# Performance work log

Hardware: AMD Instinct MI355X
Metric: run time of the kernel (lower is better)

The kernel has to match this reference:

```python
import jax, jax.numpy as jnp
import numpy as np

B, H, S, D = 4, 32, 2048, 128  # batch, heads, seq_len, d_head
D_MODEL = H * D


def setup_inputs() -> dict:
    key = jax.random.key(0)
    ks = jax.random.split(key, 6)
    return {
        "query_states": jax.random.normal(ks[0], (B, H, S, D), dtype=jnp.float32),
        "key_states": jax.random.normal(ks[1], (B, H, S, D), dtype=jnp.float32),
        "value_states": jax.random.normal(ks[2], (B, H, S, D), dtype=jnp.float32),
        "local_attn_outputs": jax.random.normal(ks[3], (B, H, S, D), dtype=jnp.float32),
        "balance_factors": jax.random.normal(ks[4], (H,), dtype=jnp.float32),
        "w_o": jax.random.normal(ks[5], (D_MODEL, D_MODEL), dtype=jnp.float32) / np.sqrt(D_MODEL),
    }


def reference(query_states, key_states, value_states, local_attn_outputs, balance_factors, w_o):
    # --- compressive memory from keys/values (elu+1 feature map) ---
    phi_k = jax.nn.elu(key_states) + 1.0                                  # [B,H,S,D]
    memory = jnp.einsum("bhsk,bhsv->bhkv", phi_k, value_states)           # [B,H,D,D]
    normalization = jnp.sum(phi_k, axis=2)                                # [B,H,D]

    # --- retrieval with query feature map, normalized ---
    phi_q = jax.nn.elu(query_states) + 1.0                                # [B,H,S,D]
    retrieved = jnp.einsum("bhsk,bhkv->bhsv", phi_q, memory)              # [B,H,S,D]
    denom = jnp.einsum("bhsk,bhk->bhs", phi_q, normalization)             # [B,H,S]
    retrieved = retrieved / denom[..., None]

    # --- sigmoid-gated combine of global (memory) and local attention ---
    gw = jax.nn.sigmoid(balance_factors)[None, :, None, None]             # global weights
    lw = jax.nn.sigmoid(1.0 - balance_factors)[None, :, None, None]      # local weights
    attn = gw * retrieved + lw * local_attn_outputs                       # [B,H,S,D]

    # [B,H,S,D] -> [B,S,H*D]
    attn = jnp.transpose(attn, (0, 2, 1, 3)).reshape(B, S, H * D)
    # o_proj: bias-free Linear, y = x @ W^T
    return attn @ w_o.T
```

## Files before the change

kernel.cpp:

```cpp
#include <hip/hip_runtime.h>
#include <hip/hip_bf16.h>

#define B_ 4
#define H_ 32
#define S_ 2048
#define D_ 128
#define DM_ 4096
#define BH_ (B_*H_)
#define M_ (B_*S_)

typedef short bf16x8 __attribute__((ext_vector_type(8)));
typedef short s16x4  __attribute__((ext_vector_type(4)));
typedef float f32x4  __attribute__((ext_vector_type(4)));

__device__ __forceinline__ float phi_f(float x) {
    return x > 0.f ? x + 1.f : __expf(x);
}

__device__ __forceinline__ short f2b(float x) {
    __hip_bfloat16 h = __float2bfloat16(x);
    return *(short*)&h;
}

__device__ __forceinline__ void gl_lds16(void* lds_uniform, const void* gptr) {
    __builtin_amdgcn_global_load_lds(
        (const __attribute__((address_space(1))) void*)gptr,
        (__attribute__((address_space(3))) void*)lds_uniform,
        16, 0, 0);
}

__global__ __launch_bounds__(256) void k1_memory(
    const float* __restrict__ Kin, const float* __restrict__ Vin,
    float* __restrict__ parts, float* __restrict__ nrmP)
{
    const int split = blockIdx.x;
    const int bh = blockIdx.y;
    const int t = threadIdx.x;
    const int wave = t >> 6, lane = t & 63;
    const int lm = lane & 15, quad = lane >> 4;
    const int wm = wave >> 1, wn = wave & 1;

    __shared__ __hip_bfloat16 sVt[128*72];
    __shared__ __hip_bfloat16 sKt[128*72];

    const long base = (long)bh * S_ * D_ + (long)split * (S_/8) * D_;
    const float* Kp = Kin + base;
    const float* Vp = Vin + base;

    f32x4 acc[4][4];
#pragma unroll
    for (int i = 0; i < 4; ++i)
#pragma unroll
        for (int j = 0; j < 4; ++j) { f32x4 z = {0.f,0.f,0.f,0.f}; acc[i][j] = z; }

    float na[2][4] = {{0.f,0.f,0.f,0.f},{0.f,0.f,0.f,0.f}};

    const int si  = t & 15;
    const int dj0 = t >> 4;

    for (int c = 0; c < 4; ++c) {
        const int s0 = c*64 + si*4;
        __syncthreads();
#pragma unroll
        for (int m = 0; m < 2; ++m) {
            const int dj = dj0 + 16*m;
            const float* gK = Kp + (long)s0*D_ + dj*4;
            const float* gV = Vp + (long)s0*D_ + dj*4;
            float4 krv[4], vrv[4];
#pragma unroll
            for (int r = 0; r < 4; ++r) {
                krv[r] = *(const float4*)(gK + (long)r*D_);
                vrv[r] = *(const float4*)(gV + (long)r*D_);
            }
            const float* kf = (const float*)krv;
            const float* vf = (const float*)vrv;
#pragma unroll
            for (int cc = 0; cc < 4; ++cc) {
                float p0 = phi_f(kf[0*4+cc]), p1 = phi_f(kf[1*4+cc]);
                float p2 = phi_f(kf[2*4+cc]), p3 = phi_f(kf[3*4+cc]);
                na[m][cc] += p0 + p1 + p2 + p3;
                s16x4 pw; pw[0]=f2b(p0); pw[1]=f2b(p1); pw[2]=f2b(p2); pw[3]=f2b(p3);
                s16x4 vw; vw[0]=f2b(vf[0*4+cc]); vw[1]=f2b(vf[1*4+cc]);
                          vw[2]=f2b(vf[2*4+cc]); vw[3]=f2b(vf[3*4+cc]);
                const int d = dj*4 + cc;
                *(s16x4*)(sKt + d*72 + si*4) = pw;
                *(s16x4*)(sVt + d*72 + si*4) = vw;
            }
        }
        __syncthreads();
#pragma unroll
        for (int kh = 0; kh < 2; ++kh) {
            const int scol = kh*32 + quad*8;
            bf16x8 af[4], bfr[4];
#pragma unroll
            for (int x = 0; x < 4; ++x) {
                af[x]  = *(const bf16x8*)(sVt + (wm*64 + x*16 + lm)*72 + scol);
                bfr[x] = *(const bf16x8*)(sKt + (wn*64 + x*16 + lm)*72 + scol);
            }
#pragma unroll
            for (int mt = 0; mt < 4; ++mt)
#pragma unroll
                for (int nt = 0; nt < 4; ++nt)
                    acc[mt][nt] = __builtin_amdgcn_mfma_f32_16x16x32_bf16(
                        af[mt], bfr[nt], acc[mt][nt], 0, 0, 0);
        }
    }

#pragma unroll
    for (int m = 0; m < 2; ++m)
#pragma unroll
        for (int cc = 0; cc < 4; ++cc) {
            float v = na[m][cc];
            v += __shfl_xor(v, 1); v += __shfl_xor(v, 2);
            v += __shfl_xor(v, 4); v += __shfl_xor(v, 8);
            na[m][cc] = v;
        }
    if (si == 0) {
        float* np = nrmP + ((long)split*BH_ + bh)*D_;
        *(float4*)&np[dj0*4]      = make_float4(na[0][0], na[0][1], na[0][2], na[0][3]);
        *(float4*)&np[(dj0+16)*4] = make_float4(na[1][0], na[1][1], na[1][2], na[1][3]);
    }

    float* mp = parts + ((long)split*BH_ + bh) * (D_*D_);
#pragma unroll
    for (int mt = 0; mt < 4; ++mt)
#pragma unroll
        for (int nt = 0; nt < 4; ++nt) {
            const int kcol = wn*64 + nt*16 + lm;
#pragma unroll
            for (int r = 0; r < 4; ++r) {
                const int vrow = wm*64 + mt*16 + quad*4 + r;
                mp[vrow*D_ + kcol] = acc[mt][nt][r];
            }
        }
}

__global__ __launch_bounds__(256) void k1b_finalize(
    const float* __restrict__ parts, const float* __restrict__ nrmP,
    __hip_bfloat16* __restrict__ memTb, float* __restrict__ nrm)
{
    const int bid = blockIdx.x;
    if (bid >= 1024) {
        const int idx = (bid - 1024)*256 + threadIdx.x;
        float s = 0.f;
#pragma unroll
        for (int sp = 0; sp < 8; ++sp) s += nrmP[(long)sp*BH_*D_ + idx];
        nrm[idx] = s;
        return;
    }
    const long g = (long)bid*256 + threadIdx.x;
    const int bh  = (int)(g >> 11);
    const int rem = (int)(g & 2047);
    const int row = rem >> 4, seg = rem & 15;
    const int srcSeg = seg ^ (row & 15);
    const long sbase = (long)bh*(D_*D_) + row*D_ + srcSeg*8;

    f32x4 s0 = {0.f,0.f,0.f,0.f}, s1 = {0.f,0.f,0.f,0.f};
#pragma unroll
    for (int sp = 0; sp < 8; ++sp) {
        const float* p = parts + (long)sp*BH_*(D_*D_) + sbase;
        s0 += *(const f32x4*)p;
        s1 += *(const f32x4*)(p + 4);
    }
    bf16x8 ob;
#pragma unroll
    for (int j = 0; j < 4; ++j) { ob[j] = f2b(s0[j]); ob[4+j] = f2b(s1[j]); }
    *(bf16x8*)(memTb + g*8) = ob;
}

__global__ __launch_bounds__(256) void k2_retrieve(
    const float* __restrict__ Qin, const float* __restrict__ Lin,
    const float* __restrict__ bal,
    const __hip_bfloat16* __restrict__ memTb, const float* __restrict__ nrm,
    __hip_bfloat16* __restrict__ attnB)
{
    const int sc = blockIdx.x;
    const int bh = blockIdx.y;
    const int b = bh >> 5, h = bh & 31;
    const int t = threadIdx.x;
    const int wave = t >> 6, lane = t & 63;
    const int lm = lane & 15, quad = lane >> 4;
    const int wm = wave >> 1, wn = wave & 1;

    __shared__ char smem[128*132*4];
    __hip_bfloat16* sQ = (__hip_bfloat16*)smem;
    __hip_bfloat16* sM = (__hip_bfloat16*)(smem + 32768);
    float* sOut = (float*)smem;
    __shared__ float sDenP[128][8];
    __shared__ float sDen[128];

    const float* Qp = Qin + (long)bh*S_*D_ + (long)sc*128*D_;
    const float* Lp = Lin + (long)bh*S_*D_ + (long)sc*128*D_;
    const __hip_bfloat16* mb = memTb + (long)bh*(D_*D_);

#pragma unroll
    for (int i = 0; i < 8; ++i)
        gl_lds16((void*)(sM + (i*256 + wave*64)*8),
                 (const void*)(mb + (long)(i*256 + wave*64 + lane)*8));

    const int kq = t & 31;
    const float4 nq = *(const float4*)(nrm + bh*D_ + kq*4);
#pragma unroll
    for (int i = 0; i < 16; ++i) {
        const int idx = t + i*256;
        const int row = idx >> 5;
        float4 qv = *(const float4*)(Qp + (long)idx*4);
        float p0 = phi_f(qv.x), p1 = phi_f(qv.y), p2 = phi_f(qv.z), p3 = phi_f(qv.w);
        float part = p0*nq.x + p1*nq.y + p2*nq.z + p3*nq.w;
        part += __shfl_xor(part, 1);
        part += __shfl_xor(part, 2);
        if ((kq & 3) == 0) sDenP[row][kq >> 2] = part;
        const int seg = kq >> 1, half = kq & 1;
        const int off = row*128 + ((seg ^ (row & 15)) << 3) + half*4;
        s16x4 qw; qw[0]=f2b(p0); qw[1]=f2b(p1); qw[2]=f2b(p2); qw[3]=f2b(p3);
        *(s16x4*)(sQ + off) = qw;
    }
    __syncthreads();

    if (t < 128) {
        float d = 0.f;
#pragma unroll
        for (int j = 0; j < 8; ++j) d += sDenP[t][j];
        sDen[t] = d;
    }

    f32x4 acc[4][4];
#pragma unroll
    for (int i = 0; i < 4; ++i)
#pragma unroll
        for (int j = 0; j < 4; ++j) { f32x4 z = {0.f,0.f,0.f,0.f}; acc[i][j] = z; }

#pragma unroll
    for (int kh = 0; kh < 4; ++kh) {
        const int segk = kh*4 + quad;
        bf16x8 af[4], bfr[4];
#pragma unroll
        for (int x = 0; x < 4; ++x) {
            const int srow = wm*64 + x*16 + lm;
            af[x]  = *(const bf16x8*)(sQ + srow*128 + ((segk ^ (srow & 15)) << 3));
            const int vrow = wn*64 + x*16 + lm;
            bfr[x] = *(const bf16x8*)(sM + vrow*128 + ((segk ^ (vrow & 15)) << 3));
        }
#pragma unroll
        for (int mt = 0; mt < 4; ++mt)
#pragma unroll
            for (int nt = 0; nt < 4; ++nt)
                acc[mt][nt] = __builtin_amdgcn_mfma_f32_16x16x32_bf16(
                    af[mt], bfr[nt], acc[mt][nt], 0, 0, 0);
    }

    const float bv = bal[h];
    const float gw = 1.f/(1.f+__expf(-bv));
    const float lw = 1.f/(1.f+__expf(-(1.f-bv)));

    __syncthreads();
#pragma unroll
    for (int mt = 0; mt < 4; ++mt)
#pragma unroll
        for (int r = 0; r < 4; ++r) {
            const int srow = wm*64 + mt*16 + quad*4 + r;
            const float scale = gw / sDen[srow];
#pragma unroll
            for (int nt = 0; nt < 4; ++nt)
                sOut[srow*132 + wn*64 + nt*16 + lm] = acc[mt][nt][r]*scale;
        }
    __syncthreads();

    const int seg = t & 15;
#pragma unroll
    for (int i = 0; i < 8; ++i) {
        const int row = (t >> 4) + i*16;
        const float* Lr = Lp + (long)row*D_ + seg*8;
        const float* Or = sOut + row*132 + seg*8;
        float4 l0 = *(const float4*)Lr;
        float4 l1 = *(const float4*)(Lr + 4);
        f32x4 o0 = *(const f32x4*)Or;
        f32x4 o1 = *(const f32x4*)(Or + 4);
        bf16x8 ob;
        ob[0] = f2b(o0[0] + lw*l0.x); ob[1] = f2b(o0[1] + lw*l0.y);
        ob[2] = f2b(o0[2] + lw*l0.z); ob[3] = f2b(o0[3] + lw*l0.w);
        ob[4] = f2b(o1[0] + lw*l1.x); ob[5] = f2b(o1[1] + lw*l1.y);
        ob[6] = f2b(o1[2] + lw*l1.z); ob[7] = f2b(o1[3] + lw*l1.w);
        const long oidx = ((long)b*S_ + sc*128 + row)*DM_ + h*D_ + seg*8;
        *(bf16x8*)(attnB + oidx) = ob;
    }
}

__global__ __launch_bounds__(256) void kconv(
    const float* __restrict__ w, __hip_bfloat16* __restrict__ wb)
{
    const long base = (long)blockIdx.x*256 + threadIdx.x;
#pragma unroll
    for (int it = 0; it < 8; ++it) {
        long i = (base + (long)it*524288)*4;
        float4 f = *(const float4*)(w + i);
        __hip_bfloat16 ob[4] = {__float2bfloat16(f.x), __float2bfloat16(f.y),
                                __float2bfloat16(f.z), __float2bfloat16(f.w)};
        *(uint2*)(wb + i) = *(uint2*)ob;
    }
}

#define GBM 256
#define GBN 256
#define GBK 64
#define GNT (DM_/GBK)

__device__ __forceinline__ bf16x8 ldfrag(const __hip_bfloat16* base, int row, int k) {
    const int kk = k ^ ((row & 7) << 3);
    return *(const bf16x8*)(base + row * GBK + kk);
}

__device__ __forceinline__ void stage_half(
    const __hip_bfloat16* __restrict__ G, __hip_bfloat16* sb,
    int r0g, int kb, int wave, int lane)
{
#pragma unroll
    for (int r = 0; r < 4; ++r) {
        const int c   = r * 512 + wave * 64 + lane;
        const int row = c >> 3;
        const int ko  = ((c & 7) ^ (row & 7)) * 8;
        gl_lds16((void*)(sb + (r * 512 + wave * 64) * 8),
                 (const void*)(G + (long)(r0g + row) * DM_ + kb + ko));
    }
}

__global__ __launch_bounds__(512, 2) void k3_gemm(
    const __hip_bfloat16* __restrict__ X,
    const __hip_bfloat16* __restrict__ W,
    float* __restrict__ Y)
{
    __shared__ alignas(16) __hip_bfloat16 sA[2][GBM * GBK];
    __shared__ alignas(16) __hip_bfloat16 sB[2][GBN * GBK];

    const int tid = threadIdx.x;
    const int wave = tid >> 6, lane = tid & 63;
    const int lm = lane & 15, quad = lane >> 4;
    const int wm = wave >> 2, wn = wave & 3;

    const int orig = blockIdx.x;
    const int wg = (orig & 7) * 64 + (orig >> 3);
    const int m0 = (wg >> 4) * GBM;
    const int n0 = (wg & 15) * GBN;

    f32x4 acc[8][4];
#pragma unroll
    for (int i = 0; i < 8; ++i)
#pragma unroll
        for (int j = 0; j < 4; ++j) { f32x4 z = {0.f,0.f,0.f,0.f}; acc[i][j] = z; }

    const int ar0 = wm * 128 + lm;
    const int br0 = wn * 64 + lm;
    const int kq  = quad * 8;

    stage_half(W, sB[0], n0, 0, wave, lane);
    stage_half(X, sA[0], m0, 0, wave, lane);
    stage_half(W, sB[1], n0, GBK, wave, lane);
    stage_half(X, sA[1], m0, GBK, wave, lane);
    asm volatile("s_waitcnt vmcnt(8)" ::: "memory");
    __builtin_amdgcn_s_barrier();

    bf16x8 a[4][2], b[4][2];

    for (int t = 0; t < GNT; ++t) {
        const int cur = t & 1;
        const __hip_bfloat16* As = sA[cur];
        const __hip_bfloat16* Bs = sB[cur];

#pragma unroll
        for (int mf = 0; mf < 4; ++mf)
#pragma unroll
            for (int kh = 0; kh < 2; ++kh)
                a[mf][kh] = ldfrag(As, ar0 + mf * 16, kh * 32 + kq);
#pragma unroll
        for (int nf = 0; nf < 4; ++nf)
#pragma unroll
            for (int kh = 0; kh < 2; ++kh)
                b[nf][kh] = ldfrag(Bs, br0 + nf * 16, kh * 32 + kq);

        __builtin_amdgcn_s_setprio(1);
#pragma unroll
        for (int mf = 0; mf < 4; ++mf)
#pragma unroll
            for (int nf = 0; nf < 4; ++nf)
#pragma unroll
                for (int kh = 0; kh < 2; ++kh)
                    acc[mf][nf] = __builtin_amdgcn_mfma_f32_16x16x32_bf16(
                        a[mf][kh], b[nf][kh], acc[mf][nf], 0, 0, 0);
        __builtin_amdgcn_s_setprio(0);

#pragma unroll
        for (int mf = 0; mf < 4; ++mf)
#pragma unroll
            for (int kh = 0; kh < 2; ++kh)
                a[mf][kh] = ldfrag(As, ar0 + 64 + mf * 16, kh * 32 + kq);

        asm volatile("s_waitcnt lgkmcnt(0)" ::: "memory");
        __builtin_amdgcn_sched_barrier(0);
        __builtin_amdgcn_s_barrier();

        if (t + 2 < GNT) {
            stage_half(W, sB[cur], n0, (t + 2) * GBK, wave, lane);
            stage_half(X, sA[cur], m0, (t + 2) * GBK, wave, lane);
        }

        __builtin_amdgcn_s_setprio(1);
#pragma unroll
        for (int mf = 0; mf < 4; ++mf)
#pragma unroll
            for (int nf = 0; nf < 4; ++nf)
#pragma unroll
                for (int kh = 0; kh < 2; ++kh)
                    acc[4 + mf][nf] = __builtin_amdgcn_mfma_f32_16x16x32_bf16(
                        a[mf][kh], b[nf][kh], acc[4 + mf][nf], 0, 0, 0);
        __builtin_amdgcn_s_setprio(0);

        if (t + 2 < GNT)
            asm volatile("s_waitcnt vmcnt(8)" ::: "memory");
        else
            asm volatile("s_waitcnt vmcnt(0)" ::: "memory");
        __builtin_amdgcn_s_barrier();
    }

#pragma unroll
    for (int mf = 0; mf < 8; ++mf) {
        const int row = m0 + wm * 128 + mf * 16 + quad * 4;
#pragma unroll
        for (int nf = 0; nf < 4; ++nf) {
            const int col = n0 + wn * 64 + nf * 16 + lm;
#pragma unroll
            for (int r = 0; r < 4; ++r)
                Y[(long)(row + r) * DM_ + col] = acc[mf][nf][r];
        }
    }
}

extern "C" void kernel_launch(void* const* d_in, const int* in_sizes, int n_in,
                              void* d_out, int out_size, void* d_ws, size_t ws_size,
                              hipStream_t stream) {
    const float* Q   = (const float*)d_in[0];
    const float* K   = (const float*)d_in[1];
    const float* V   = (const float*)d_in[2];
    const float* L   = (const float*)d_in[3];
    const float* bal = (const float*)d_in[4];
    const float* Wo  = (const float*)d_in[5];
    float* Y = (float*)d_out;

    char* ws = (char*)d_ws;
    float* parts = (float*)ws;
    __hip_bfloat16* attnB = (__hip_bfloat16*)ws;
    __hip_bfloat16* woB = (__hip_bfloat16*)(ws + 67108864);
    float* nrm   = (float*)(ws + 100663296);
    __hip_bfloat16* memTb = (__hip_bfloat16*)(ws + 100728832);
    float* nrmP  = (float*)(ws + 104923136);


    k1_memory<<<dim3(8, BH_), 256, 0, stream>>>(K, V, parts, nrmP);
    k1b_finalize<<<1088, 256, 0, stream>>>(parts, nrmP, memTb, nrm);
    kconv<<<2048, 256, 0, stream>>>(Wo, woB);
    k2_retrieve<<<dim3(S_/128, BH_), 256, 0, stream>>>(Q, L, bal, memTb, nrm, attnB);
    k3_gemm<<<dim3(512), 512, 0, stream>>>(attnB, woB, Y);
}
```

Baseline: 829.6 us.

## Load W fragments directly from global and halve GEMM tile N

The output-projection GEMM stops staging the weight tile through LDS. Each wave now reads its B fragments straight from global memory into registers, and only the activation tile is double-buffered in LDS. The block tile shrinks from 256x256 with 512 threads to 256x128 with 256 threads, doubling the grid. This saves LDS space and barrier traffic but makes the B loads uncoalesced and unpipelined, and the vmcnt(8) waits no longer match the mix of outstanding global loads.

```diff
diff --git a/kernel.cpp b/kernel.cpp
--- a/kernel.cpp
+++ b/kernel.cpp
@@ -301,46 +301,45 @@
 }
 
 #define GBM 256
-#define GBN 256
+#define GBN 128
 #define GBK 64
 #define GNT (DM_/GBK)
 
-__device__ __forceinline__ bf16x8 ldfrag(const __hip_bfloat16* base, int row, int k) {
+__device__ __forceinline__ bf16x8 ldfragA(const __hip_bfloat16* base, int row, int k) {
     const int kk = k ^ ((row & 7) << 3);
     return *(const bf16x8*)(base + row * GBK + kk);
 }
 
-__device__ __forceinline__ void stage_half(
-    const __hip_bfloat16* __restrict__ G, __hip_bfloat16* sb,
-    int r0g, int kb, int wave, int lane)
-{
-#pragma unroll
-    for (int r = 0; r < 4; ++r) {
-        const int c   = r * 512 + wave * 64 + lane;
+__device__ __forceinline__ void stageA(
+    const __hip_bfloat16* __restrict__ X, __hip_bfloat16* sb,
+    int m0, int kb, int wave, int lane, int t)
+{
+#pragma unroll
+    for (int r = 0; r < 8; ++r) {
+        const int c   = r * 256 + t;
         const int row = c >> 3;
         const int ko  = ((c & 7) ^ (row & 7)) * 8;
-        gl_lds16((void*)(sb + (r * 512 + wave * 64) * 8),
-                 (const void*)(G + (long)(r0g + row) * DM_ + kb + ko));
-    }
-}
-
-__global__ __launch_bounds__(512, 2) void k3_gemm(
+        gl_lds16((void*)(sb + (r * 256 + wave * 64) * 8),
+                 (const void*)(X + (long)(m0 + row) * DM_ + kb + ko));
+    }
+}
+
+__global__ __launch_bounds__(256, 2) void k3_gemm(
     const __hip_bfloat16* __restrict__ X,
     const __hip_bfloat16* __restrict__ W,
     float* __restrict__ Y)
 {
     __shared__ alignas(16) __hip_bfloat16 sA[2][GBM * GBK];
-    __shared__ alignas(16) __hip_bfloat16 sB[2][GBN * GBK];
-
-    const int tid = threadIdx.x;
-    const int wave = tid >> 6, lane = tid & 63;
+
+    const int t = threadIdx.x;
+    const int wave = t >> 6, lane = t & 63;
     const int lm = lane & 15, quad = lane >> 4;
-    const int wm = wave >> 2, wn = wave & 3;
+    const int wm = wave >> 1, wn = wave & 1;
 
     const int orig = blockIdx.x;
-    const int wg = (orig & 7) * 64 + (orig >> 3);
-    const int m0 = (wg >> 4) * GBM;
-    const int n0 = (wg & 15) * GBN;
+    const int wg = (orig & 7) * 128 + (orig >> 3);
+    const int m0 = (wg >> 5) * GBM;
+    const int n0 = (wg & 31) * GBN;
 
     f32x4 acc[8][4];
 #pragma unroll
@@ -349,33 +348,32 @@
         for (int j = 0; j < 4; ++j) { f32x4 z = {0.f,0.f,0.f,0.f}; acc[i][j] = z; }
 
     const int ar0 = wm * 128 + lm;
-    const int br0 = wn * 64 + lm;
+    const long bn0 = n0 + wn * 64 + lm;
     const int kq  = quad * 8;
 
-    stage_half(W, sB[0], n0, 0, wave, lane);
-    stage_half(X, sA[0], m0, 0, wave, lane);
-    stage_half(W, sB[1], n0, GBK, wave, lane);
-    stage_half(X, sA[1], m0, GBK, wave, lane);
+    stageA(X, sA[0], m0, 0, wave, lane, t);
+    stageA(X, sA[1], m0, GBK, wave, lane, t);
     asm volatile("s_waitcnt vmcnt(8)" ::: "memory");
     __builtin_amdgcn_s_barrier();
 
     bf16x8 a[4][2], b[4][2];
 
-    for (int t = 0; t < GNT; ++t) {
-        const int cur = t & 1;
+    for (int tt = 0; tt < GNT; ++tt) {
+        const int cur = tt & 1;
         const __hip_bfloat16* As = sA[cur];
-        const __hip_bfloat16* Bs = sB[cur];
+        const int kb = tt * GBK;
+
+#pragma unroll
+        for (int nf = 0; nf < 4; ++nf)
+#pragma unroll
+            for (int kh = 0; kh < 2; ++kh)
+                b[nf][kh] = *(const bf16x8*)(W + (bn0 + nf * 16) * DM_ + kb + kh * 32 + kq);
 
 #pragma unroll
         for (int mf = 0; mf < 4; ++mf)
 #pragma unroll
             for (int kh = 0; kh < 2; ++kh)
-                a[mf][kh] = ldfrag(As, ar0 + mf * 16, kh * 32 + kq);
-#pragma unroll
-        for (int nf = 0; nf < 4; ++nf)
-#pragma unroll
-            for (int kh = 0; kh < 2; ++kh)
-                b[nf][kh] = ldfrag(Bs, br0 + nf * 16, kh * 32 + kq);
+                a[mf][kh] = ldfragA(As, ar0 + mf * 16, kh * 32 + kq);
 
         __builtin_amdgcn_s_setprio(1);
 #pragma unroll
@@ -392,16 +390,14 @@
         for (int mf = 0; mf < 4; ++mf)
 #pragma unroll
             for (int kh = 0; kh < 2; ++kh)
-                a[mf][kh] = ldfrag(As, ar0 + 64 + mf * 16, kh * 32 + kq);
+                a[mf][kh] = ldfragA(As, ar0 + 64 + mf * 16, kh * 32 + kq);
 
         asm volatile("s_waitcnt lgkmcnt(0)" ::: "memory");
         __builtin_amdgcn_sched_barrier(0);
         __builtin_amdgcn_s_barrier();
 
-        if (t + 2 < GNT) {
-            stage_half(W, sB[cur], n0, (t + 2) * GBK, wave, lane);
-            stage_half(X, sA[cur], m0, (t + 2) * GBK, wave, lane);
-        }
+        if (tt + 2 < GNT)
+            stageA(X, sA[cur], m0, (tt + 2) * GBK, wave, lane, t);
 
         __builtin_amdgcn_s_setprio(1);
 #pragma unroll
@@ -414,7 +410,7 @@
                         a[mf][kh], b[nf][kh], acc[4 + mf][nf], 0, 0, 0);
         __builtin_amdgcn_s_setprio(0);
 
-        if (t + 2 < GNT)
+        if (tt + 2 < GNT)
             asm volatile("s_waitcnt vmcnt(8)" ::: "memory");
         else
             asm volatile("s_waitcnt vmcnt(0)" ::: "memory");
@@ -453,10 +449,9 @@
     __hip_bfloat16* memTb = (__hip_bfloat16*)(ws + 100728832);
     float* nrmP  = (float*)(ws + 104923136);
 
-
     k1_memory<<<dim3(8, BH_), 256, 0, stream>>>(K, V, parts, nrmP);
     k1b_finalize<<<1088, 256, 0, stream>>>(parts, nrmP, memTb, nrm);
     kconv<<<2048, 256, 0, stream>>>(Wo, woB);
     k2_retrieve<<<dim3(S_/128, BH_), 256, 0, stream>>>(Q, L, bal, memTb, nrm, attnB);
-    k3_gemm<<<dim3(512), 512, 0, stream>>>(attnB, woB, Y);
-}
+    k3_gemm<<<dim3(1024), 256, 0, stream>>>(attnB, woB, Y);
+}
```

Result: slower. 910.4 us (+9.7%).
